# Performance work log

Measured on AMD Instinct MI355X. Metric: run time of the kernel, lower is better.

Reference implementation:

```python
import jax, jax.numpy as jnp
import numpy as np

TOKENS_PER_LAYER = 16  # v in rearrange 'b l (a v) -> b l a v'


def setup_inputs() -> dict:
    key = jax.random.key(0)
    k1, k2 = jax.random.split(key)
    vocab, embed_dim = 1024, 256
    x = jax.random.normal(k1, (64, 32, embed_dim * TOKENS_PER_LAYER), dtype=jnp.float32)
    # nn.Embedding init: uniform(-1/vocab, 1/vocab)
    emb_weight = jax.random.uniform(k2, (vocab, embed_dim), dtype=jnp.float32,
                                    minval=-1.0 / vocab, maxval=1.0 / vocab)
    return {"x": x, "emb_weight": emb_weight}


def reference(x, emb_weight):
    v = TOKENS_PER_LAYER
    b, l, av = x.shape
    a = av // v  # embed_dim
    # rearrange 'b l (a v) -> b l a v'
    z = x.reshape(b, l, a, v)
    # rearrange 'b l a v -> (b l v) a'
    z_flat = z.transpose(0, 1, 3, 2).reshape(b * l * v, a)
    # pairwise squared L2 distance via sum-of-squares + GEMM: [N, vocab]
    dist = (jnp.sum(z_flat * z_flat, axis=1, keepdims=True)
            + jnp.sum(emb_weight * emb_weight, axis=1)
            - 2.0 * (z_flat @ emb_weight.T))
    tokens = jnp.argmin(dist, axis=-1)  # [N] int
    # embedding gather, then rearrange '(b l v) e -> b l e v'
    z_q = emb_weight[tokens].reshape(b, l, v, a).transpose(0, 1, 3, 2)
    # straight-through decoder input: z + sg(z_q - z)
    decoder_input = z + jax.lax.stop_gradient(z_q - z)
    tokens = tokens.reshape(b, l, v)
    return z_q, decoder_input, tokens
```

## Files before the change

### kernel.cpp

```cpp
#include <hip/hip_runtime.h>


#define A_DIM 256
#define VOCAB 1024
#define NROWS 32768
#define ZQ_ELEMS ((size_t)8388608)
#define TAU_C 3.0e-4f
#define TAU_F 2.0e-4f

typedef _Float16 f16x8 __attribute__((ext_vector_type(8)));
typedef float f32x4 __attribute__((ext_vector_type(4)));

#define WS_EHT   ((size_t)0)
#define WS_ZH    ((size_t)524288)
#define WS_ESQ   ((size_t)17301504)
#define WS_ZSQ   ((size_t)17305600)
#define WS_TOK   ((size_t)17436672)
#define WS_PLIST ((size_t)17567744)
#define WS_FLIST ((size_t)18092032)
#define WS_CNT   ((size_t)18223104)
#define WS_NEED  ((size_t)18223232)


__global__ __launch_bounds__(256) void prep_e_kernel(const float* __restrict__ emb,
                                                     float* __restrict__ esq,
                                                     _Float16* __restrict__ eht,
                                                     int* __restrict__ cnt) {
    int j = blockIdx.x * 256 + threadIdx.x;
    if (blockIdx.x == 0 && threadIdx.x < 2) cnt[threadIdx.x] = 0;
    if (j >= VOCAB) return;
    const float4* row = (const float4*)(emb + (size_t)j * A_DIM);
    double s = 0.0;
    #pragma unroll 4
    for (int t = 0; t < A_DIM / 4; ++t) {
        float4 f = row[t];
        float sx = f.x * f.x, sy = f.y * f.y, sz = f.z * f.z, sw = f.w * f.w;
        s += (double)sx + (double)sy + (double)sz + (double)sw;
    }
    esq[j] = (float)s;
    #pragma unroll 4
    for (int kb = 0; kb < 32; ++kb) {
        float4 e0 = row[kb * 2], e1 = row[kb * 2 + 1];
        f16x8 h;
        h[0] = (_Float16)e0.x; h[1] = (_Float16)e0.y; h[2] = (_Float16)e0.z; h[3] = (_Float16)e0.w;
        h[4] = (_Float16)e1.x; h[5] = (_Float16)e1.y; h[6] = (_Float16)e1.z; h[7] = (_Float16)e1.w;
        *(f16x8*)(eht + ((size_t)kb * 1024 + j) * 8) = h;
    }
}

__global__ __launch_bounds__(256) void prep_z_kernel(const float* __restrict__ x,
                                                     _Float16* __restrict__ zh,
                                                     float* __restrict__ zsq) {
    __shared__ float raw[A_DIM * 17];
    const int tid = threadIdx.x;
    const int bl = blockIdx.x;
    #pragma unroll
    for (int t = 0; t < 4; ++t) {
        int f4 = tid * 4 + t * 1024;
        float4 val = *(const float4*)(x + (size_t)bl * 4096 + f4);
        int a = f4 >> 4, v0 = f4 & 15;
        raw[a * 17 + v0 + 0] = val.x;
        raw[a * 17 + v0 + 1] = val.y;
        raw[a * 17 + v0 + 2] = val.z;
        raw[a * 17 + v0 + 3] = val.w;
    }
    __syncthreads();
    #pragma unroll
    for (int t = 0; t < 16; ++t) {
        int f = tid + t * 256;
        int v = f >> 8, a = f & 255;
        zh[((size_t)bl * 16 + v) * 256 + a] = (_Float16)raw[a * 17 + v];
    }
    if (tid < 16) {
        double s = 0.0;
        for (int a = 0; a < A_DIM; ++a) {
            float zf = raw[a * 17 + tid];
            float z2 = zf * zf;
            s += (double)z2;
        }
        zsq[bl * 16 + tid] = (float)s;
    }
}

__global__ __launch_bounds__(256, 2) void mfma_kernel(const _Float16* __restrict__ zh,
                                                      const _Float16* __restrict__ eht,
                                                      const float* __restrict__ esq_g,
                                                      int* __restrict__ tok,
                                                      int4* __restrict__ plist,
                                                      int* __restrict__ flist,
                                                      int* __restrict__ cnt,
                                                      float* __restrict__ out) {
    const int tid = threadIdx.x;
    const int w = tid >> 6;
    const int lane = tid & 63;
    const int q = lane >> 4;
    const int ln = lane & 15;
    const int row0 = blockIdx.x * 64 + w * 16;

    f16x8 afr[8];
    #pragma unroll
    for (int kt = 0; kt < 8; ++kt)
        afr[kt] = *(const f16x8*)(zh + (size_t)(row0 + ln) * 256 + kt * 32 + q * 8);

    float tv1[4], tv2[4], tv3[4];
    int   ti1[4], ti2[4], ti3[4];
    #pragma unroll
    for (int s = 0; s < 4; ++s) {
        tv1[s] = 3.0e38f; tv2[s] = 3.0e38f; tv3[s] = 3.0e38f;
        ti1[s] = 0; ti2[s] = 0; ti3[s] = 0;
    }

    #define LOAD_CHUNK(c0, bfr)                                                          \
        {                                                                                \
            _Pragma("unroll")                                                            \
            for (int kt = 0; kt < 8; ++kt)                                               \
                bfr[kt] = *(const f16x8*)(eht +                                          \
                    ((size_t)(kt * 4 + q) * 1024 + (c0) + ln) * 8);                      \
        }

    #define COMPUTE_CHUNK(c0, bfr)                                                       \
        {                                                                                \
            f32x4 acc = (f32x4){0.f, 0.f, 0.f, 0.f};                                     \
            _Pragma("unroll")                                                            \
            for (int kt = 0; kt < 8; ++kt)                                               \
                acc = __builtin_amdgcn_mfma_f32_16x16x32_f16(afr[kt], bfr[kt], acc,      \
                                                             0, 0, 0);                   \
            const int cand = (c0) + ln;                                                  \
            float es = esq_g[cand];                                                      \
            _Pragma("unroll")                                                            \
            for (int reg = 0; reg < 4; ++reg) {                                          \
                float s = fmaf(-2.0f, acc[reg], es);                                     \
                if (s < tv3[reg]) {                                                      \
                    if (s < tv2[reg]) {                                                  \
                        tv3[reg] = tv2[reg]; ti3[reg] = ti2[reg];                        \
                        if (s < tv1[reg]) {                                              \
                            tv2[reg] = tv1[reg]; ti2[reg] = ti1[reg];                    \
                            tv1[reg] = s; ti1[reg] = cand;                               \
                        } else { tv2[reg] = s; ti2[reg] = cand; }                        \
                    } else { tv3[reg] = s; ti3[reg] = cand; }                            \
                }                                                                        \
            }                                                                            \
        }

    f16x8 bA[8], bB[8];
    LOAD_CHUNK(0, bA)
    for (int ch = 0; ch < 64; ch += 2) {
        LOAD_CHUNK((ch + 1) * 16, bB)
        COMPUTE_CHUNK(ch * 16, bA)
        if (ch + 2 < 64) LOAD_CHUNK((ch + 2) * 16, bA)
        COMPUTE_CHUNK((ch + 1) * 16, bB)
    }
    #undef LOAD_CHUNK
    #undef COMPUTE_CHUNK

    #pragma unroll
    for (int slot = 0; slot < 4; ++slot) {
        float v1 = tv1[slot], v2 = tv2[slot], v3 = tv3[slot];
        int i1 = ti1[slot], i2 = ti2[slot], i3 = ti3[slot];
        #pragma unroll
        for (int m = 1; m <= 8; m <<= 1) {
            float ov1 = __shfl_xor(v1, m); int oi1 = __shfl_xor(i1, m);
            float ov2 = __shfl_xor(v2, m); int oi2 = __shfl_xor(i2, m);
            float ov3 = __shfl_xor(v3, m); int oi3 = __shfl_xor(i3, m);
            #define INS3(ov, oi)                                                         \
                if (ov < v3 || (ov == v3 && oi < i3)) {                                  \
                    if (ov < v2 || (ov == v2 && oi < i2)) {                              \
                        v3 = v2; i3 = i2;                                                \
                        if (ov < v1 || (ov == v1 && oi < i1)) {                          \
                            v2 = v1; i2 = i1; v1 = ov; i1 = oi;                          \
                        } else { v2 = ov; i2 = oi; }                                     \
                    } else { v3 = ov; i3 = oi; }                                         \
                }
            INS3(ov1, oi1)
            INS3(ov2, oi2)
            INS3(ov3, oi3)
            #undef INS3
        }
        if (ln == 0) {
            int row = row0 + q * 4 + slot;
            tok[row] = i1;
            out[2 * ZQ_ELEMS + (size_t)row] = (float)i1;
            if (v2 - v1 <= TAU_C) {
                if (v3 - v1 > TAU_C) {
                    int p = atomicAdd(&cnt[0], 1) & (NROWS - 1);
                    plist[p] = make_int4(row, i1, i2, 0);
                } else {
                    int p = atomicAdd(&cnt[1], 1) & (NROWS - 1);
                    flist[p] = row;
                }
            }
        }
    }
}

__global__ __launch_bounds__(256) void rescan2_kernel(const float* __restrict__ x,
                                                      const float* __restrict__ emb,
                                                      const float* __restrict__ esq,
                                                      const float* __restrict__ zsq,
                                                      int* __restrict__ tok,
                                                      const int4* __restrict__ plist,
                                                      const int* __restrict__ flist,
                                                      const int* __restrict__ cnt,
                                                      float* __restrict__ out) {
    __shared__ float zrow[A_DIM];
    __shared__ float wv[4];
    __shared__ int   wi[4];
    const int tid = threadIdx.x;
    const int w = tid >> 6, lane = tid & 63;

    {
        const int nw = gridDim.x * 4;
        const int gw = blockIdx.x * 4 + w;
        const int np = min(cnt[0], NROWS);
        for (int i = gw; i < np; i += nw) {
            int4 e = plist[i];
            const int r = e.x, c1 = e.y, c2 = e.z;
            const float* xr = x + (size_t)(r >> 4) * 4096 + (r & 15);
            const float* e1 = emb + (size_t)c1 * A_DIM;
            const float* e2 = emb + (size_t)c2 * A_DIM;
            double d1 = 0.0, d2 = 0.0;
            #pragma unroll
            for (int k = 0; k < 4; ++k) {
                int a = lane + k * 64;
                double zv = (double)xr[a * 16];
                d1 = fma(zv, (double)e1[a], d1);
                d2 = fma(zv, (double)e2[a], d2);
            }
            #pragma unroll
            for (int m = 1; m < 64; m <<= 1) {
                d1 += __shfl_xor(d1, m);
                d2 += __shfl_xor(d2, m);
            }
            if (lane == 0) {
                float zq = zsq[r];
                float A1 = zq + esq[c1];
                float D1 = (float)(2.0 * d1);
                float s1 = A1 - D1;
                float A2 = zq + esq[c2];
                float D2 = (float)(2.0 * d2);
                float s2 = A2 - D2;
                int bi = (s2 < s1 || (s2 == s1 && c2 < c1)) ? c2 : c1;
                tok[r] = bi;
                out[2 * ZQ_ELEMS + (size_t)r] = (float)bi;
            }
        }
    }

    const int nf = min(cnt[1], NROWS);
    for (int i = blockIdx.x; i < nf; i += gridDim.x) {
        const int r = flist[i];
        __syncthreads();
        zrow[tid] = x[(size_t)(r >> 4) * 4096 + (size_t)tid * 16 + (r & 15)];
        __syncthreads();

        const float4* e0 = (const float4*)(emb + (size_t)tid * 4 * A_DIM);
        double d0 = 0.0, d1 = 0.0, d2 = 0.0, d3 = 0.0;
        #pragma unroll 8
        for (int k4 = 0; k4 < A_DIM / 4; ++k4) {
            float4 zf = *(const float4*)&zrow[k4 * 4];
            double z0 = (double)zf.x, z1 = (double)zf.y;
            double z2 = (double)zf.z, z3 = (double)zf.w;
            float4 f0 = e0[k4];
            float4 f1 = e0[64 + k4];
            float4 f2 = e0[128 + k4];
            float4 f3 = e0[192 + k4];
            d0 = fma((double)f0.x, z0, d0); d0 = fma((double)f0.y, z1, d0);
            d0 = fma((double)f0.z, z2, d0); d0 = fma((double)f0.w, z3, d0);
            d1 = fma((double)f1.x, z0, d1); d1 = fma((double)f1.y, z1, d1);
            d1 = fma((double)f1.z, z2, d1); d1 = fma((double)f1.w, z3, d1);
            d2 = fma((double)f2.x, z0, d2); d2 = fma((double)f2.y, z1, d2);
            d2 = fma((double)f2.z, z2, d2); d2 = fma((double)f2.w, z3, d2);
            d3 = fma((double)f3.x, z0, d3); d3 = fma((double)f3.y, z1, d3);
            d3 = fma((double)f3.z, z2, d3); d3 = fma((double)f3.w, z3, d3);
        }
        const float zq = zsq[r];
        float bv = 3.0e38f; int bi = 0;
        double dd[4] = {d0, d1, d2, d3};
        #pragma unroll
        for (int cc = 0; cc < 4; ++cc) {
            int c = tid * 4 + cc;
            float A = zq + esq[c];
            float D = (float)(2.0 * dd[cc]);
            float s = A - D;
            if (s < bv) { bv = s; bi = c; }
        }
        #pragma unroll
        for (int m = 1; m < 64; m <<= 1) {
            float ov = __shfl_xor(bv, m); int oi = __shfl_xor(bi, m);
            if (ov < bv || (ov == bv && oi < bi)) { bv = ov; bi = oi; }
        }
        if (lane == 0) { wv[w] = bv; wi[w] = bi; }
        __syncthreads();
        if (tid == 0) {
            float BV = wv[0]; int BI = wi[0];
            #pragma unroll
            for (int t = 1; t < 4; ++t)
                if (wv[t] < BV || (wv[t] == BV && wi[t] < BI)) { BV = wv[t]; BI = wi[t]; }
            tok[r] = BI;
            out[2 * ZQ_ELEMS + (size_t)r] = (float)BI;
        }
    }
}

__global__ __launch_bounds__(256) void gather_kernel(const float* __restrict__ emb,
                                                     const int* __restrict__ tok,
                                                     float* __restrict__ out) {
    __shared__ int t16[16];
    const int tid = threadIdx.x;
    const int bl = blockIdx.x;
    if (tid < 16) t16[tid] = tok[bl * 16 + tid];
    __syncthreads();
    const int a = tid;
    __align__(16) float h[16];
    #pragma unroll
    for (int v = 0; v < 16; ++v) h[v] = emb[(size_t)t16[v] * A_DIM + a];
    size_t base = ((size_t)bl * A_DIM + a) * 16;
    float4* p0 = (float4*)(out + base);
    float4* p1 = (float4*)(out + ZQ_ELEMS + base);
    #pragma unroll
    for (int qq = 0; qq < 4; ++qq) {
        float4 val = *(float4*)&h[qq * 4];
        p0[qq] = val;
        p1[qq] = val;
    }
}


__global__ __launch_bounds__(256) void prep_f(const float* __restrict__ emb,
                                              float* __restrict__ e_sq32) {
    int j = blockIdx.x * 256 + threadIdx.x;
    if (j < VOCAB) {
        const float4* row = (const float4*)(emb + (size_t)j * A_DIM);
        double s = 0.0;
        #pragma unroll 4
        for (int t = 0; t < A_DIM / 4; ++t) {
            float4 f = row[t];
            float sx = f.x * f.x, sy = f.y * f.y, sz = f.z * f.z, sw = f.w * f.w;
            s += (double)sx + (double)sy + (double)sz + (double)sw;
        }
        e_sq32[j] = (float)s;
    }
}

#define FBM 64
#define FBN 256
#define FBK 32
struct SmemF {
    union {
        struct { float zs[FBK][FBM]; float es[FBK][FBN]; };
        float4 mbuf[FBM][32];
        struct { double zrow[A_DIM]; float rbest[256]; int ridx[256]; };
    };
    double zsqp_s[4][FBM];
    float  zsq[FBM];
    int    tok[FBM];
    int    flagrows[FBM];
    int    nflag;
};

__global__ __launch_bounds__(256, 2) void main_f(const float* __restrict__ x,
                                                 const float* __restrict__ emb,
                                                 const float* __restrict__ e_sq32,
                                                 float* __restrict__ out) {
    __shared__ SmemF sm;
    const int tid = threadIdx.x;
    const int tx = tid & 31;
    const int ty = tid >> 5;
    const int blk = blockIdx.x;
    const int row0 = blk * FBM;
    const int bl0 = row0 >> 4;
    const int zrow_id = tid & 63;
    const int zq4     = tid >> 6;

    if (tid == 0) sm.nflag = 0;
    float v1[8], v2[8];
    int   i1[8], i2[8];
    #pragma unroll
    for (int r = 0; r < 8; ++r) { v1[r] = 3.0e38f; v2[r] = 3.0e38f; i1[r] = 0; i2[r] = 0; }
    double zsqp = 0.0;
    float4 zpf[2];
    float4 epf[8];
    for (int ct = 0; ct < VOCAB / FBN; ++ct) {
        float acc[8][8];
        #pragma unroll
        for (int rr = 0; rr < 8; ++rr)
            #pragma unroll
            for (int cc = 0; cc < 8; ++cc) acc[rr][cc] = 0.0f;
        for (int kt = 0; kt < A_DIM / FBK; ++kt) {
            if (kt == 0) {
                #pragma unroll
                for (int t = 0; t < 2; ++t) {
                    int f = tid + t * 256;
                    int v4 = f & 3, g = (f >> 2) & 3, kk = f >> 4;
                    zpf[t] = *(const float4*)(x + (size_t)(bl0 + g) * 4096 + (kt * FBK + kk) * 16 + v4 * 4);
                }
                #pragma unroll
                for (int t = 0; t < 8; ++t) {
                    int f = tid + t * 256;
                    int c = f & 255, k4 = f >> 8;
                    epf[t] = *(const float4*)(emb + (size_t)(ct * FBN + c) * A_DIM + kt * FBK + k4 * 4);
                }
            }
            __syncthreads();
            #pragma unroll
            for (int t = 0; t < 2; ++t) {
                int f = tid + t * 256;
                int v4 = f & 3, g = (f >> 2) & 3, kk = f >> 4;
                *(float4*)&sm.zs[kk][g * 16 + v4 * 4] = zpf[t];
            }
            #pragma unroll
            for (int t = 0; t < 8; ++t) {
                int f = tid + t * 256;
                int c = f & 255, k4 = f >> 8;
                sm.es[k4 * 4 + 0][c] = epf[t].x;
                sm.es[k4 * 4 + 1][c] = epf[t].y;
                sm.es[k4 * 4 + 2][c] = epf[t].z;
                sm.es[k4 * 4 + 3][c] = epf[t].w;
            }
            __syncthreads();
            if (kt + 1 < A_DIM / FBK) {
                #pragma unroll
                for (int t = 0; t < 2; ++t) {
                    int f = tid + t * 256;
                    int v4 = f & 3, g = (f >> 2) & 3, kk = f >> 4;
                    zpf[t] = *(const float4*)(x + (size_t)(bl0 + g) * 4096 + ((kt + 1) * FBK + kk) * 16 + v4 * 4);
                }
                #pragma unroll
                for (int t = 0; t < 8; ++t) {
                    int f = tid + t * 256;
                    int c = f & 255, k4 = f >> 8;
                    epf[t] = *(const float4*)(emb + (size_t)(ct * FBN + c) * A_DIM + (kt + 1) * FBK + k4 * 4);
                }
            }
            if (ct == 0 && (kt >> 1) == zq4) {
                #pragma unroll
                for (int kk = 0; kk < FBK; ++kk) {
                    float zf = sm.zs[kk][zrow_id];
                    float zf2 = zf * zf;
                    zsqp += (double)zf2;
                }
            }
            #pragma unroll 2
            for (int kk = 0; kk < FBK; ++kk) {
                float4 za = *(float4*)&sm.zs[kk][ty * 4];
                float4 zb = *(float4*)&sm.zs[kk][32 + ty * 4];
                float4 ea = *(float4*)&sm.es[kk][tx * 4];
                float4 eb = *(float4*)&sm.es[kk][128 + tx * 4];
                float zv[8] = {za.x, za.y, za.z, za.w, zb.x, zb.y, zb.z, zb.w};
                float ev[8] = {ea.x, ea.y, ea.z, ea.w, eb.x, eb.y, eb.z, eb.w};
                #pragma unroll
                for (int rr = 0; rr < 8; ++rr)
                    #pragma unroll
                    for (int cc = 0; cc < 8; ++cc)
                        acc[rr][cc] = fmaf(zv[rr], ev[cc], acc[rr][cc]);
            }
        }
        if (ct == 0) {
            sm.zsqp_s[zq4][zrow_id] = zsqp;
            __syncthreads();
            if (tid < FBM)
                sm.zsq[tid] = (float)(sm.zsqp_s[0][tid] + sm.zsqp_s[1][tid]
                                    + sm.zsqp_s[2][tid] + sm.zsqp_s[3][tid]);
            __syncthreads();
        }
        float esqv[8];
        #pragma unroll
        for (int cc = 0; cc < 8; ++cc) {
            int c = ct * FBN + (cc >> 2) * 128 + tx * 4 + (cc & 3);
            esqv[cc] = e_sq32[c];
        }
        #pragma unroll
        for (int rr = 0; rr < 8; ++rr) {
            int R = (rr >> 2) * 32 + ty * 4 + (rr & 3);
            float zq = sm.zsq[R];
            #pragma unroll
            for (int cc = 0; cc < 8; ++cc) {
                int c = ct * FBN + (cc >> 2) * 128 + tx * 4 + (cc & 3);
                float A = zq + esqv[cc];
                float s = fmaf(-2.0f, acc[rr][cc], A);
                if (s < v1[rr]) { v2[rr] = v1[rr]; i2[rr] = i1[rr]; v1[rr] = s; i1[rr] = c; }
                else if (s < v2[rr]) { v2[rr] = s; i2[rr] = c; }
            }
        }
    }
    __syncthreads();
    #pragma unroll
    for (int rr = 0; rr < 8; ++rr) {
        int r = (rr >> 2) * 32 + ty * 4 + (rr & 3);
        float4 m;
        m.x = v1[rr]; m.y = __int_as_float(i1[rr]);
        m.z = v2[rr]; m.w = __int_as_float(i2[rr]);
        sm.mbuf[r][tx] = m;
    }
    __syncthreads();
    if (tid < FBM) {
        int r = tid;
        float V1 = 3.0e38f, V2 = 3.0e38f;
        int I1 = 0, I2 = 0;
        for (int t = 0; t < 32; ++t) {
            float4 m = sm.mbuf[r][t];
            float a1 = m.x; int a1i = __float_as_int(m.y);
            float a2 = m.z; int a2i = __float_as_int(m.w);
            if (a1 < V1 || (a1 == V1 && a1i < I1)) { V2 = V1; I2 = I1; V1 = a1; I1 = a1i; }
            else if (a1 < V2 || (a1 == V2 && a1i < I2)) { V2 = a1; I2 = a1i; }
            if (a2 < V1 || (a2 == V1 && a2i < I1)) { V2 = V1; I2 = I1; V1 = a2; I1 = a2i; }
            else if (a2 < V2 || (a2 == V2 && a2i < I2)) { V2 = a2; I2 = a2i; }
        }
        sm.tok[r] = I1;
        if (V2 - V1 <= TAU_F) {
            int pos = atomicAdd(&sm.nflag, 1);
            sm.flagrows[pos] = r;
        }
    }
    __syncthreads();
    const int nf = sm.nflag;
    for (int i = 0; i < nf; ++i) {
        const int rl = sm.flagrows[i];
        const int bl = bl0 + (rl >> 4);
        const int v  = rl & 15;
        const float zqrow = sm.zsq[rl];
        sm.zrow[tid] = (double)x[(size_t)bl * 4096 + (size_t)tid * 16 + v];
        __syncthreads();
        float bv = 3.0e38f; int bi = 0;
        #pragma unroll
        for (int cc = 0; cc < 4; ++cc) {
            int c = tid * 4 + cc;
            const float4* er = (const float4*)(emb + (size_t)c * A_DIM);
            double dot = 0.0;
            #pragma unroll 8
            for (int k4 = 0; k4 < A_DIM / 4; ++k4) {
                float4 f = er[k4];
                dot = fma((double)f.x, sm.zrow[k4 * 4 + 0], dot);
                dot = fma((double)f.y, sm.zrow[k4 * 4 + 1], dot);
                dot = fma((double)f.z, sm.zrow[k4 * 4 + 2], dot);
                dot = fma((double)f.w, sm.zrow[k4 * 4 + 3], dot);
            }
            float A = zqrow + e_sq32[c];
            float D = (float)(2.0 * dot);
            float s = A - D;
            if (s < bv) { bv = s; bi = c; }
        }
        sm.rbest[tid] = bv; sm.ridx[tid] = bi;
        __syncthreads();
        if (tid == 0) {
            float BV = sm.rbest[0]; int BI = sm.ridx[0];
            for (int t = 1; t < 256; ++t) {
                float vv = sm.rbest[t];
                if (vv < BV) { BV = vv; BI = sm.ridx[t]; }
            }
            sm.tok[rl] = BI;
        }
        __syncthreads();
    }
    if (tid < FBM) {
        out[2 * ZQ_ELEMS + (size_t)(row0 + tid)] = (float)sm.tok[tid];
    }
    __syncthreads();
    const int a = tid;
    for (int g = 0; g < 4; ++g) {
        __align__(16) float h[16];
        #pragma unroll
        for (int v = 0; v < 16; ++v) {
            h[v] = emb[(size_t)sm.tok[g * 16 + v] * A_DIM + a];
        }
        size_t base = ((size_t)(bl0 + g) * A_DIM + a) * 16;
        float4* p0 = (float4*)(out + base);
        float4* p1 = (float4*)(out + ZQ_ELEMS + base);
        #pragma unroll
        for (int qq = 0; qq < 4; ++qq) {
            float4 val = *(float4*)&h[qq * 4];
            p0[qq] = val;
            p1[qq] = val;
        }
    }
}

extern "C" void kernel_launch(void* const* d_in, const int* in_sizes, int n_in,
                              void* d_out, int out_size, void* d_ws, size_t ws_size,
                              hipStream_t stream) {
    (void)in_sizes; (void)n_in; (void)out_size;
    const float* x   = (const float*)d_in[0];
    const float* emb = (const float*)d_in[1];
    float* out = (float*)d_out;
    char* ws = (char*)d_ws;

    if (ws_size >= WS_NEED) {
        _Float16* eht = (_Float16*)(ws + WS_EHT);
        _Float16* zh  = (_Float16*)(ws + WS_ZH);
        float* esq    = (float*)(ws + WS_ESQ);
        float* zsq    = (float*)(ws + WS_ZSQ);
        int* tok      = (int*)(ws + WS_TOK);
        int4* plist   = (int4*)(ws + WS_PLIST);
        int* flist    = (int*)(ws + WS_FLIST);
        int* cnt      = (int*)(ws + WS_CNT);

        prep_e_kernel<<<4, 256, 0, stream>>>(emb, esq, eht, cnt);
        prep_z_kernel<<<2048, 256, 0, stream>>>(x, zh, zsq);
        mfma_kernel<<<512, 256, 0, stream>>>(zh, eht, esq, tok, plist, flist, cnt, out);
        rescan2_kernel<<<256, 256, 0, stream>>>(x, emb, esq, zsq, tok, plist, flist, cnt, out);
        gather_kernel<<<2048, 256, 0, stream>>>(emb, tok, out);
    } else {
        float* e_sq32 = (float*)ws;
        prep_f<<<4, 256, 0, stream>>>(emb, e_sq32);
        main_f<<<512, 256, 0, stream>>>(x, emb, e_sq32, out);
    }
}
```

Measured before the change: 252.8 us.

## Split vocab across waves in MFMA argmin kernel and parallelize codebook prep

The MFMA distance kernel now gives each block 32 rows instead of 64. Each pair of waves covers one half of the vocabulary, and the two partial top-3 lists are merged through shared memory before tokens and rescan lists are written. This doubles the grid size to raise parallelism, and splits the MFMA accumulation into two independent chains to shorten dependency latency. It drops the explicit double-buffered B loads and the occupancy hint, and adds a block-wide sync. The codebook prep kernel also spreads the fp16 conversion across 16 threads per row over 64 blocks instead of one thread per row.

```diff
diff --git a/kernel.cpp b/kernel.cpp
--- a/kernel.cpp
+++ b/kernel.cpp
@@ -26,25 +26,29 @@
                                                      float* __restrict__ esq,
                                                      _Float16* __restrict__ eht,
                                                      int* __restrict__ cnt) {
-    int j = blockIdx.x * 256 + threadIdx.x;
-    if (blockIdx.x == 0 && threadIdx.x < 2) cnt[threadIdx.x] = 0;
-    if (j >= VOCAB) return;
+    const int tid = threadIdx.x;
+    if (blockIdx.x == 0 && tid < 2) cnt[tid] = 0;
+    const int j = blockIdx.x * 16 + (tid & 15);
+    const int sub = tid >> 4;
     const float4* row = (const float4*)(emb + (size_t)j * A_DIM);
-    double s = 0.0;
-    #pragma unroll 4
-    for (int t = 0; t < A_DIM / 4; ++t) {
-        float4 f = row[t];
-        float sx = f.x * f.x, sy = f.y * f.y, sz = f.z * f.z, sw = f.w * f.w;
-        s += (double)sx + (double)sy + (double)sz + (double)sw;
-    }
-    esq[j] = (float)s;
-    #pragma unroll 4
-    for (int kb = 0; kb < 32; ++kb) {
+    #pragma unroll
+    for (int t = 0; t < 2; ++t) {
+        int kb = sub * 2 + t;
         float4 e0 = row[kb * 2], e1 = row[kb * 2 + 1];
         f16x8 h;
         h[0] = (_Float16)e0.x; h[1] = (_Float16)e0.y; h[2] = (_Float16)e0.z; h[3] = (_Float16)e0.w;
         h[4] = (_Float16)e1.x; h[5] = (_Float16)e1.y; h[6] = (_Float16)e1.z; h[7] = (_Float16)e1.w;
         *(f16x8*)(eht + ((size_t)kb * 1024 + j) * 8) = h;
+    }
+    if (sub == 0) {
+        double s = 0.0;
+        #pragma unroll 4
+        for (int t = 0; t < A_DIM / 4; ++t) {
+            float4 f = row[t];
+            float sx = f.x * f.x, sy = f.y * f.y, sz = f.z * f.z, sw = f.w * f.w;
+            s += (double)sx + (double)sy + (double)sz + (double)sw;
+        }
+        esq[j] = (float)s;
     }
 }
 
@@ -82,25 +86,34 @@
     }
 }
 
-__global__ __launch_bounds__(256, 2) void mfma_kernel(const _Float16* __restrict__ zh,
-                                                      const _Float16* __restrict__ eht,
-                                                      const float* __restrict__ esq_g,
-                                                      int* __restrict__ tok,
-                                                      int4* __restrict__ plist,
-                                                      int* __restrict__ flist,
-                                                      int* __restrict__ cnt,
-                                                      float* __restrict__ out) {
+__global__ __launch_bounds__(256) void mfma_kernel(const _Float16* __restrict__ zh,
+                                                   const _Float16* __restrict__ eht,
+                                                   const float* __restrict__ esq_g,
+                                                   int* __restrict__ tok,
+                                                   int4* __restrict__ plist,
+                                                   int* __restrict__ flist,
+                                                   int* __restrict__ cnt,
+                                                   float* __restrict__ out) {
+    __shared__ float t3buf[2][32][6];
     const int tid = threadIdx.x;
     const int w = tid >> 6;
     const int lane = tid & 63;
     const int q = lane >> 4;
     const int ln = lane & 15;
-    const int row0 = blockIdx.x * 64 + w * 16;
+    const int g = w & 1;
+    const int h = w >> 1;
+    const int row0 = blockIdx.x * 32 + g * 16;
+    const int cbase = h * 512;
 
     f16x8 afr[8];
     #pragma unroll
     for (int kt = 0; kt < 8; ++kt)
         afr[kt] = *(const f16x8*)(zh + (size_t)(row0 + ln) * 256 + kt * 32 + q * 8);
+
+    const f16x8* ep[8];
+    #pragma unroll
+    for (int kt = 0; kt < 8; ++kt)
+        ep[kt] = (const f16x8*)(eht + ((size_t)(kt * 4 + q) * 1024 + cbase + ln) * 8);
 
     float tv1[4], tv2[4], tv3[4];
     int   ti1[4], ti2[4], ti3[4];
@@ -110,48 +123,35 @@
         ti1[s] = 0; ti2[s] = 0; ti3[s] = 0;
     }
 
-    #define LOAD_CHUNK(c0, bfr)                                                          \
-        {                                                                                \
-            _Pragma("unroll")                                                            \
-            for (int kt = 0; kt < 8; ++kt)                                               \
-                bfr[kt] = *(const f16x8*)(eht +                                          \
-                    ((size_t)(kt * 4 + q) * 1024 + (c0) + ln) * 8);                      \
-        }
-
-    #define COMPUTE_CHUNK(c0, bfr)                                                       \
-        {                                                                                \
-            f32x4 acc = (f32x4){0.f, 0.f, 0.f, 0.f};                                     \
-            _Pragma("unroll")                                                            \
-            for (int kt = 0; kt < 8; ++kt)                                               \
-                acc = __builtin_amdgcn_mfma_f32_16x16x32_f16(afr[kt], bfr[kt], acc,      \
-                                                             0, 0, 0);                   \
-            const int cand = (c0) + ln;                                                  \
-            float es = esq_g[cand];                                                      \
-            _Pragma("unroll")                                                            \
-            for (int reg = 0; reg < 4; ++reg) {                                          \
-                float s = fmaf(-2.0f, acc[reg], es);                                     \
-                if (s < tv3[reg]) {                                                      \
-                    if (s < tv2[reg]) {                                                  \
-                        tv3[reg] = tv2[reg]; ti3[reg] = ti2[reg];                        \
-                        if (s < tv1[reg]) {                                              \
-                            tv2[reg] = tv1[reg]; ti2[reg] = ti1[reg];                    \
-                            tv1[reg] = s; ti1[reg] = cand;                               \
-                        } else { tv2[reg] = s; ti2[reg] = cand; }                        \
-                    } else { tv3[reg] = s; ti3[reg] = cand; }                            \
-                }                                                                        \
-            }                                                                            \
-        }
-
-    f16x8 bA[8], bB[8];
-    LOAD_CHUNK(0, bA)
-    for (int ch = 0; ch < 64; ch += 2) {
-        LOAD_CHUNK((ch + 1) * 16, bB)
-        COMPUTE_CHUNK(ch * 16, bA)
-        if (ch + 2 < 64) LOAD_CHUNK((ch + 2) * 16, bA)
-        COMPUTE_CHUNK((ch + 1) * 16, bB)
-    }
-    #undef LOAD_CHUNK
-    #undef COMPUTE_CHUNK
+    for (int ch = 0; ch < 32; ++ch) {
+        f16x8 bfr[8];
+        #pragma unroll
+        for (int kt = 0; kt < 8; ++kt)
+            bfr[kt] = ep[kt][(size_t)ch * 16];
+        f32x4 a0 = (f32x4){0.f, 0.f, 0.f, 0.f};
+        f32x4 a1 = (f32x4){0.f, 0.f, 0.f, 0.f};
+        #pragma unroll
+        for (int kt = 0; kt < 4; ++kt)
+            a0 = __builtin_amdgcn_mfma_f32_16x16x32_f16(afr[kt], bfr[kt], a0, 0, 0, 0);
+        #pragma unroll
+        for (int kt = 4; kt < 8; ++kt)
+            a1 = __builtin_amdgcn_mfma_f32_16x16x32_f16(afr[kt], bfr[kt], a1, 0, 0, 0);
+        const int cand = cbase + ch * 16 + ln;
+        float es = esq_g[cand];
+        #pragma unroll
+        for (int reg = 0; reg < 4; ++reg) {
+            float s = fmaf(-2.0f, a0[reg] + a1[reg], es);
+            if (s < tv3[reg]) {
+                if (s < tv2[reg]) {
+                    tv3[reg] = tv2[reg]; ti3[reg] = ti2[reg];
+                    if (s < tv1[reg]) {
+                        tv2[reg] = tv1[reg]; ti2[reg] = ti1[reg];
+                        tv1[reg] = s; ti1[reg] = cand;
+                    } else { tv2[reg] = s; ti2[reg] = cand; }
+                } else { tv3[reg] = s; ti3[reg] = cand; }
+            }
+        }
+    }
 
     #pragma unroll
     for (int slot = 0; slot < 4; ++slot) {
@@ -177,17 +177,43 @@
             #undef INS3
         }
         if (ln == 0) {
-            int row = row0 + q * 4 + slot;
-            tok[row] = i1;
-            out[2 * ZQ_ELEMS + (size_t)row] = (float)i1;
-            if (v2 - v1 <= TAU_C) {
-                if (v3 - v1 > TAU_C) {
-                    int p = atomicAdd(&cnt[0], 1) & (NROWS - 1);
-                    plist[p] = make_int4(row, i1, i2, 0);
-                } else {
-                    int p = atomicAdd(&cnt[1], 1) & (NROWS - 1);
-                    flist[p] = row;
-                }
+            int rl = g * 16 + q * 4 + slot;
+            float* hp = &t3buf[h][rl][0];
+            hp[0] = v1; hp[1] = __int_as_float(i1);
+            hp[2] = v2; hp[3] = __int_as_float(i2);
+            hp[4] = v3; hp[5] = __int_as_float(i3);
+        }
+    }
+    __syncthreads();
+
+    if (tid < 32) {
+        const float* h0 = &t3buf[0][tid][0];
+        const float* h1 = &t3buf[1][tid][0];
+        float v1 = h0[0]; int i1 = __float_as_int(h0[1]);
+        float v2 = h0[2]; int i2 = __float_as_int(h0[3]);
+        float v3 = h0[4]; int i3 = __float_as_int(h0[5]);
+        #pragma unroll
+        for (int e = 0; e < 3; ++e) {
+            float ov = h1[2 * e]; int oi = __float_as_int(h1[2 * e + 1]);
+            if (ov < v3 || (ov == v3 && oi < i3)) {
+                if (ov < v2 || (ov == v2 && oi < i2)) {
+                    v3 = v2; i3 = i2;
+                    if (ov < v1 || (ov == v1 && oi < i1)) {
+                        v2 = v1; i2 = i1; v1 = ov; i1 = oi;
+                    } else { v2 = ov; i2 = oi; }
+                } else { v3 = ov; i3 = oi; }
+            }
+        }
+        int row = blockIdx.x * 32 + tid;
+        tok[row] = i1;
+        out[2 * ZQ_ELEMS + (size_t)row] = (float)i1;
+        if (v2 - v1 <= TAU_C) {
+            if (v3 - v1 > TAU_C) {
+                int p = atomicAdd(&cnt[0], 1) & (NROWS - 1);
+                plist[p] = make_int4(row, i1, i2, 0);
+            } else {
+                int p = atomicAdd(&cnt[1], 1) & (NROWS - 1);
+                flist[p] = row;
             }
         }
     }
@@ -594,9 +620,9 @@
         int* flist    = (int*)(ws + WS_FLIST);
         int* cnt      = (int*)(ws + WS_CNT);
 
-        prep_e_kernel<<<4, 256, 0, stream>>>(emb, esq, eht, cnt);
+        prep_e_kernel<<<64, 256, 0, stream>>>(emb, esq, eht, cnt);
         prep_z_kernel<<<2048, 256, 0, stream>>>(x, zh, zsq);
-        mfma_kernel<<<512, 256, 0, stream>>>(zh, eht, esq, tok, plist, flist, cnt, out);
+        mfma_kernel<<<1024, 256, 0, stream>>>(zh, eht, esq, tok, plist, flist, cnt, out);
         rescan2_kernel<<<256, 256, 0, stream>>>(x, emb, esq, zsq, tok, plist, flist, cnt, out);
         gather_kernel<<<2048, 256, 0, stream>>>(emb, tok, out);
     } else {
```

Result: faster. 230.8 us (-8.7%).
